# Kernel optimization log

Hardware: AMD Instinct MI355X
Metric: run time of the kernel (lower is better)

Reference implementation:

```python
import jax, jax.numpy as jnp
import numpy as np

SIGMA = 5.0
KSIZE = 31  # int(6*sigma+1), odd
CHANNEL = 3

def build_gaussian_kernel(size, sigma):
    coords = jnp.arange(size, dtype=jnp.float32) - size // 2
    g = jnp.exp(-coords ** 2 / (2.0 * sigma ** 2))
    g = g / g.sum()
    k2d = g[:, None] * g[None, :]            # (k, k)
    # depthwise kernel: (O=C, I/g=1, k, k)
    return jnp.broadcast_to(k2d[None, None], (CHANNEL, 1, size, size))

def depthwise_blur(x, kernel):
    # x: (B, C, H, W); kernel: (C, 1, k, k); groups = C, SAME-style padding k//2
    pad = KSIZE // 2
    return jax.lax.conv_general_dilated(
        x, kernel,
        window_strides=(1, 1),
        padding=((pad, pad), (pad, pad)),
        dimension_numbers=("NCHW", "OIHW", "NCHW"),
        feature_group_count=CHANNEL,
    )

def setup_inputs() -> dict:
    key = jax.random.key(0)
    k1, k2 = jax.random.split(key)
    B, C, H, W = 16, 3, 512, 512
    background = jax.random.uniform(k1, (B, C, H, W), dtype=jnp.float32)
    insatance = jax.random.uniform(k2, (B, C, H, W), dtype=jnp.float32)
    gaussian_kernel = build_gaussian_kernel(KSIZE, SIGMA)
    return {"background": background, "insatance": insatance,
            "gaussian_kernel": gaussian_kernel}

def reference(background, insatance, gaussian_kernel):
    # retinex_decompose(background): only illumination1 is used downstream
    bg_log = jnp.log1p(background)
    illumination1 = depthwise_blur(bg_log, gaussian_kernel)
    # retinex_decompose(insatance): reflectance2 = log1p(ins) - blur(log1p(ins))
    ins_log = jnp.log1p(insatance)
    illumination2 = depthwise_blur(ins_log, gaussian_kernel)
    reflectance2 = ins_log - illumination2
    # adjust_illumination(reflectance2, illumination1)
    img_log = reflectance2 + illumination1
    img_corrected = jnp.clip(jnp.expm1(img_log), 0.0, 1.0)
    return img_corrected
```

## Files before the change

### kernel.cpp

```cpp
#include <hip/hip_runtime.h>


constexpr int W_ = 512, H_ = 512, NIMG = 48;
constexpr int TS = 64;
constexpr int RS = 94;
constexpr int PITCH = 68;

__device__ constexpr float G[31] = {
    8.8805851e-04f, 1.5861066e-03f, 2.7217699e-03f, 4.4874399e-03f,
    7.1084368e-03f, 1.0818767e-02f, 1.5820117e-02f, 2.2226435e-02f,
    3.0002549e-02f, 3.8911209e-02f, 4.8486352e-02f, 5.8048702e-02f,
    6.6771901e-02f, 7.3794364e-02f, 7.8357552e-02f, 7.9940480e-02f,
    7.8357552e-02f, 7.3794364e-02f, 6.6771901e-02f, 5.8048702e-02f,
    4.8486352e-02f, 3.8911209e-02f, 3.0002549e-02f, 2.2226435e-02f,
    1.5820117e-02f, 1.0818767e-02f, 7.1084368e-03f, 4.4874399e-03f,
    2.7217699e-03f, 1.5861066e-03f, 8.8805851e-04f};

__global__ __launch_bounds__(256) void vpass(const float* __restrict__ bg,
                                             const float* __restrict__ ins,
                                             float* __restrict__ tmpT) {
  __shared__ __align__(16) float sb[RS * PITCH];
  const int tid  = threadIdx.x;
  const int lane = tid & 63;
  const int w    = tid >> 6;
  const int x0 = blockIdx.x * TS, y0 = blockIdx.y * TS;
  const size_t base = (size_t)blockIdx.z * ((size_t)H_ * W_);

#pragma unroll
  for (int it = 0; it < 6; ++it) {
    const int idx = tid + 256 * it;
    if (idx < RS * 16) {
      const int r = idx >> 4, c = idx & 15;
      const int y = y0 - 15 + r;
      float4 v = make_float4(0.f, 0.f, 0.f, 0.f);
      if ((unsigned)y < (unsigned)H_) {
        const size_t a = base + (size_t)y * W_ + x0 + 4 * c;
        const float4 b = *(const float4*)(bg + a);
        const float4 n = *(const float4*)(ins + a);
        v.x = __logf(1.f + b.x) - __logf(1.f + n.x);
        v.y = __logf(1.f + b.y) - __logf(1.f + n.y);
        v.z = __logf(1.f + b.z) - __logf(1.f + n.z);
        v.w = __logf(1.f + b.w) - __logf(1.f + n.w);
      }
      *(float4*)(sb + r * PITCH + 4 * c) = v;
    }
  }
  __syncthreads();

  float acc[16];
#pragma unroll
  for (int p = 0; p < 16; ++p) acc[p] = 0.f;
#pragma unroll
  for (int j = 0; j < 46; ++j) {
    const float v = sb[(16 * w + j) * PITCH + lane];
#pragma unroll
    for (int p = 0; p < 16; ++p) {
      const int c = j - p;
      if (c >= 0 && c < 31) acc[p] += G[c] * v;
    }
  }
  __syncthreads();

  float4* st4 = (float4*)sb;
#pragma unroll
  for (int q = 0; q < 4; ++q)
    st4[lane * 17 + 4 * w + q] =
        make_float4(acc[4 * q], acc[4 * q + 1], acc[4 * q + 2], acc[4 * q + 3]);
  __syncthreads();
#pragma unroll
  for (int it = 0; it < 4; ++it) {
    const int idx = tid + 256 * it;
    const int x = idx >> 4, y4 = idx & 15;
    const float4 v = st4[x * 17 + y4];
    *(float4*)(tmpT + base + (size_t)(x0 + x) * H_ + y0 + 4 * y4) = v;
  }
}

__global__ __launch_bounds__(256) void hpass(const float* __restrict__ tmpT,
                                             const float* __restrict__ ins,
                                             float* __restrict__ out) {
  __shared__ __align__(16) float sb[RS * PITCH];
  const int tid  = threadIdx.x;
  const int lane = tid & 63;
  const int w    = tid >> 6;
  const int x0 = blockIdx.x * TS, y0 = blockIdx.y * TS;
  const size_t base = (size_t)blockIdx.z * ((size_t)H_ * W_);

#pragma unroll
  for (int it = 0; it < 6; ++it) {
    const int idx = tid + 256 * it;
    if (idx < RS * 16) {
      const int r = idx >> 4, c = idx & 15;
      const int x = x0 - 15 + r;
      float4 v = make_float4(0.f, 0.f, 0.f, 0.f);
      if ((unsigned)x < (unsigned)W_)
        v = *(const float4*)(tmpT + base + (size_t)x * H_ + y0 + 4 * c);
      *(float4*)(sb + r * PITCH + 4 * c) = v;
    }
  }
  __syncthreads();

  float acc[16];
#pragma unroll
  for (int p = 0; p < 16; ++p) acc[p] = 0.f;
#pragma unroll
  for (int j = 0; j < 46; ++j) {
    const float v = sb[(16 * w + j) * PITCH + lane];
#pragma unroll
    for (int p = 0; p < 16; ++p) {
      const int c = j - p;
      if (c >= 0 && c < 31) acc[p] += G[c] * v;
    }
  }
  __syncthreads();

  float4* st4 = (float4*)sb;
#pragma unroll
  for (int q = 0; q < 4; ++q)
    st4[lane * 17 + 4 * w + q] =
        make_float4(acc[4 * q], acc[4 * q + 1], acc[4 * q + 2], acc[4 * q + 3]);
  __syncthreads();
#pragma unroll
  for (int it = 0; it < 4; ++it) {
    const int idx = tid + 256 * it;
    const int y = idx >> 4, x4 = idx & 15;
    const float4 b = st4[y * 17 + x4];
    const size_t a = base + (size_t)(y0 + y) * W_ + x0 + 4 * x4;
    const float4 n = *(const float4*)(ins + a);
    float4 o;
    o.x = fminf(fmaxf(__expf(__logf(1.f + n.x) + b.x) - 1.f, 0.f), 1.f);
    o.y = fminf(fmaxf(__expf(__logf(1.f + n.y) + b.y) - 1.f, 0.f), 1.f);
    o.z = fminf(fmaxf(__expf(__logf(1.f + n.z) + b.z) - 1.f, 0.f), 1.f);
    o.w = fminf(fmaxf(__expf(__logf(1.f + n.w) + b.w) - 1.f, 0.f), 1.f);
    *(float4*)(out + a) = o;
  }
}

extern "C" void kernel_launch(void* const* d_in, const int* in_sizes, int n_in,
                              void* d_out, int out_size, void* d_ws, size_t ws_size,
                              hipStream_t stream) {
  const float* bg  = (const float*)d_in[0];
  const float* ins = (const float*)d_in[1];
  float* out = (float*)d_out;

  const size_t need = (size_t)NIMG * H_ * W_ * sizeof(float);
  float* tmpT = (ws_size >= need) ? (float*)d_ws : (float*)d_in[0];

  dim3 grid(W_ / TS, H_ / TS, NIMG);
  vpass<<<grid, dim3(256), 0, stream>>>(bg, ins, tmpT);
  hpass<<<grid, dim3(256), 0, stream>>>(tmpT, ins, out);
}
```

Baseline: 171.8 us.

## Enlarge tiles to 128 rows, batch global loads, drop LDS transpose on store

Both passes now use 512-thread blocks covering 64x128 tiles, which cuts the halo overhead (158 rows loaded per 128 outputs instead of 94 per 64). All global loads are issued into registers before the log and LDS writes, to raise memory-level parallelism. The LDS transpose before output is removed: each thread writes its 16 consecutive accumulators directly as float4s, saving two barriers and LDS traffic. In exchange, stores become strided across lanes, which may hurt coalescing, and the added register arrays raise register pressure under the 512-thread, 6-blocks-per-CU launch bound.

```diff
diff --git a/kernel.cpp b/kernel.cpp
--- a/kernel.cpp
+++ b/kernel.cpp
@@ -2,9 +2,9 @@
 
 
 constexpr int W_ = 512, H_ = 512, NIMG = 48;
-constexpr int TS = 64;
-constexpr int RS = 94;
+constexpr int RS = 158;
 constexpr int PITCH = 68;
+constexpr int NITEMS = RS * 16;
 
 __device__ constexpr float G[31] = {
     8.8805851e-04f, 1.5861066e-03f, 2.7217699e-03f, 4.4874399e-03f,
@@ -16,32 +16,40 @@
     1.5820117e-02f, 1.0818767e-02f, 7.1084368e-03f, 4.4874399e-03f,
     2.7217699e-03f, 1.5861066e-03f, 8.8805851e-04f};
 
-__global__ __launch_bounds__(256) void vpass(const float* __restrict__ bg,
-                                             const float* __restrict__ ins,
-                                             float* __restrict__ tmpT) {
+__global__ __launch_bounds__(512, 6) void vpass(const float* __restrict__ bg,
+                                                const float* __restrict__ ins,
+                                                float* __restrict__ tmpT) {
   __shared__ __align__(16) float sb[RS * PITCH];
-  const int tid  = threadIdx.x;
-  const int lane = tid & 63;
-  const int w    = tid >> 6;
-  const int x0 = blockIdx.x * TS, y0 = blockIdx.y * TS;
+  const int tid = threadIdx.x;
+  const int lane = tid & 63, w = tid >> 6;
+  const int x0 = blockIdx.x * 64, y0 = blockIdx.y * 128;
   const size_t base = (size_t)blockIdx.z * ((size_t)H_ * W_);
 
+  float4 bv[5], nv[5];
 #pragma unroll
-  for (int it = 0; it < 6; ++it) {
-    const int idx = tid + 256 * it;
-    if (idx < RS * 16) {
+  for (int it = 0; it < 5; ++it) {
+    const int idx = tid + 512 * it;
+    const int r = idx >> 4, c = idx & 15;
+    const int y = y0 - 15 + r;
+    const bool ok = (idx < NITEMS) && ((unsigned)y < (unsigned)H_);
+    bv[it] = make_float4(0.f, 0.f, 0.f, 0.f);
+    nv[it] = bv[it];
+    if (ok) {
+      const size_t a = base + (size_t)y * W_ + x0 + 4 * c;
+      bv[it] = *(const float4*)(bg + a);
+      nv[it] = *(const float4*)(ins + a);
+    }
+  }
+#pragma unroll
+  for (int it = 0; it < 5; ++it) {
+    const int idx = tid + 512 * it;
+    if (idx < NITEMS) {
       const int r = idx >> 4, c = idx & 15;
-      const int y = y0 - 15 + r;
-      float4 v = make_float4(0.f, 0.f, 0.f, 0.f);
-      if ((unsigned)y < (unsigned)H_) {
-        const size_t a = base + (size_t)y * W_ + x0 + 4 * c;
-        const float4 b = *(const float4*)(bg + a);
-        const float4 n = *(const float4*)(ins + a);
-        v.x = __logf(1.f + b.x) - __logf(1.f + n.x);
-        v.y = __logf(1.f + b.y) - __logf(1.f + n.y);
-        v.z = __logf(1.f + b.z) - __logf(1.f + n.z);
-        v.w = __logf(1.f + b.w) - __logf(1.f + n.w);
-      }
+      float4 v;
+      v.x = __logf(1.f + bv[it].x) - __logf(1.f + nv[it].x);
+      v.y = __logf(1.f + bv[it].y) - __logf(1.f + nv[it].y);
+      v.z = __logf(1.f + bv[it].z) - __logf(1.f + nv[it].z);
+      v.w = __logf(1.f + bv[it].w) - __logf(1.f + nv[it].w);
       *(float4*)(sb + r * PITCH + 4 * c) = v;
     }
   }
@@ -59,43 +67,40 @@
       if (c >= 0 && c < 31) acc[p] += G[c] * v;
     }
   }
-  __syncthreads();
-
-  float4* st4 = (float4*)sb;
+  {
+    float* dst = tmpT + base + (size_t)(x0 + lane) * H_ + y0 + 16 * w;
 #pragma unroll
-  for (int q = 0; q < 4; ++q)
-    st4[lane * 17 + 4 * w + q] =
-        make_float4(acc[4 * q], acc[4 * q + 1], acc[4 * q + 2], acc[4 * q + 3]);
-  __syncthreads();
-#pragma unroll
-  for (int it = 0; it < 4; ++it) {
-    const int idx = tid + 256 * it;
-    const int x = idx >> 4, y4 = idx & 15;
-    const float4 v = st4[x * 17 + y4];
-    *(float4*)(tmpT + base + (size_t)(x0 + x) * H_ + y0 + 4 * y4) = v;
+    for (int q = 0; q < 4; ++q)
+      *(float4*)(dst + 4 * q) =
+          make_float4(acc[4 * q], acc[4 * q + 1], acc[4 * q + 2], acc[4 * q + 3]);
   }
 }
 
-__global__ __launch_bounds__(256) void hpass(const float* __restrict__ tmpT,
-                                             const float* __restrict__ ins,
-                                             float* __restrict__ out) {
+__global__ __launch_bounds__(512, 6) void hpass(const float* __restrict__ tmpT,
+                                                const float* __restrict__ ins,
+                                                float* __restrict__ out) {
   __shared__ __align__(16) float sb[RS * PITCH];
-  const int tid  = threadIdx.x;
-  const int lane = tid & 63;
-  const int w    = tid >> 6;
-  const int x0 = blockIdx.x * TS, y0 = blockIdx.y * TS;
+  const int tid = threadIdx.x;
+  const int lane = tid & 63, w = tid >> 6;
+  const int x0 = blockIdx.x * 128, y0 = blockIdx.y * 64;
   const size_t base = (size_t)blockIdx.z * ((size_t)H_ * W_);
 
+  float4 tv[5];
 #pragma unroll
-  for (int it = 0; it < 6; ++it) {
-    const int idx = tid + 256 * it;
-    if (idx < RS * 16) {
+  for (int it = 0; it < 5; ++it) {
+    const int idx = tid + 512 * it;
+    const int r = idx >> 4, c = idx & 15;
+    const int x = x0 - 15 + r;
+    tv[it] = make_float4(0.f, 0.f, 0.f, 0.f);
+    if ((idx < NITEMS) && ((unsigned)x < (unsigned)W_))
+      tv[it] = *(const float4*)(tmpT + base + (size_t)x * H_ + y0 + 4 * c);
+  }
+#pragma unroll
+  for (int it = 0; it < 5; ++it) {
+    const int idx = tid + 512 * it;
+    if (idx < NITEMS) {
       const int r = idx >> 4, c = idx & 15;
-      const int x = x0 - 15 + r;
-      float4 v = make_float4(0.f, 0.f, 0.f, 0.f);
-      if ((unsigned)x < (unsigned)W_)
-        v = *(const float4*)(tmpT + base + (size_t)x * H_ + y0 + 4 * c);
-      *(float4*)(sb + r * PITCH + 4 * c) = v;
+      *(float4*)(sb + r * PITCH + 4 * c) = tv[it];
     }
   }
   __syncthreads();
@@ -112,27 +117,18 @@
       if (c >= 0 && c < 31) acc[p] += G[c] * v;
     }
   }
-  __syncthreads();
-
-  float4* st4 = (float4*)sb;
+  {
+    const size_t a0 = base + (size_t)(y0 + lane) * W_ + x0 + 16 * w;
 #pragma unroll
-  for (int q = 0; q < 4; ++q)
-    st4[lane * 17 + 4 * w + q] =
-        make_float4(acc[4 * q], acc[4 * q + 1], acc[4 * q + 2], acc[4 * q + 3]);
-  __syncthreads();
-#pragma unroll
-  for (int it = 0; it < 4; ++it) {
-    const int idx = tid + 256 * it;
-    const int y = idx >> 4, x4 = idx & 15;
-    const float4 b = st4[y * 17 + x4];
-    const size_t a = base + (size_t)(y0 + y) * W_ + x0 + 4 * x4;
-    const float4 n = *(const float4*)(ins + a);
-    float4 o;
-    o.x = fminf(fmaxf(__expf(__logf(1.f + n.x) + b.x) - 1.f, 0.f), 1.f);
-    o.y = fminf(fmaxf(__expf(__logf(1.f + n.y) + b.y) - 1.f, 0.f), 1.f);
-    o.z = fminf(fmaxf(__expf(__logf(1.f + n.z) + b.z) - 1.f, 0.f), 1.f);
-    o.w = fminf(fmaxf(__expf(__logf(1.f + n.w) + b.w) - 1.f, 0.f), 1.f);
-    *(float4*)(out + a) = o;
+    for (int q = 0; q < 4; ++q) {
+      const float4 n = *(const float4*)(ins + a0 + 4 * q);
+      float4 o;
+      o.x = fminf(fmaxf(__expf(__logf(1.f + n.x) + acc[4 * q + 0]) - 1.f, 0.f), 1.f);
+      o.y = fminf(fmaxf(__expf(__logf(1.f + n.y) + acc[4 * q + 1]) - 1.f, 0.f), 1.f);
+      o.z = fminf(fmaxf(__expf(__logf(1.f + n.z) + acc[4 * q + 2]) - 1.f, 0.f), 1.f);
+      o.w = fminf(fmaxf(__expf(__logf(1.f + n.w) + acc[4 * q + 3]) - 1.f, 0.f), 1.f);
+      *(float4*)(out + a0 + 4 * q) = o;
+    }
   }
 }
 
@@ -146,7 +142,6 @@
   const size_t need = (size_t)NIMG * H_ * W_ * sizeof(float);
   float* tmpT = (ws_size >= need) ? (float*)d_ws : (float*)d_in[0];
 
-  dim3 grid(W_ / TS, H_ / TS, NIMG);
-  vpass<<<grid, dim3(256), 0, stream>>>(bg, ins, tmpT);
-  hpass<<<grid, dim3(256), 0, stream>>>(tmpT, ins, out);
+  vpass<<<dim3(8, 4, NIMG), dim3(512), 0, stream>>>(bg, ins, tmpT);
+  hpass<<<dim3(4, 8, NIMG), dim3(512), 0, stream>>>(tmpT, ins, out);
 }
```

New measurement: 183.2 us. +6.7%, slower.
